# Optimization experiments

Measured on AMD Instinct MI355X. Metric: run time of the kernel, lower is better.

Reference implementation:

```python
import jax, jax.numpy as jnp
import numpy as np

NUM_ITERATIONS = 3


def squash(s, axis):
    # s: capsule vectors; squash along `axis` (capsule dim)
    mag_sq = jnp.sum(s * s, axis=axis, keepdims=True)
    mag = jnp.sqrt(mag_sq)
    return mag_sq / (1.0 + mag_sq) * (s / mag)


def setup_inputs() -> dict:
    key = jax.random.key(0)
    k1, k2 = jax.random.split(key)
    B, IN_SIZE, I = 256, 8, 1152   # batch, in_size, in_node_num
    N, O = 10, 16                  # num_node, node_size
    x = jax.random.normal(k1, (B, IN_SIZE, I), dtype=jnp.float32)
    W = jax.random.normal(k2, (1, I, N, O, IN_SIZE), dtype=jnp.float32)
    return {"x": x, "W": W}


def reference(x, W):
    # x: (B, in_size, I); W: (1, I, N, O, in_size)
    B = x.shape[0]
    I, N = W.shape[1], W.shape[2]
    xt = jnp.swapaxes(x, 1, 2)  # (B, I, in_size)
    # u_hat[b,i,n,o] = sum_k (0.03*W[0,i,n,o,k]) * x[b,i,k]
    u_hat = jnp.einsum('inok,bik->bino', W[0] * 0.03, xt)  # (B, I, N, O)
    b_ij = jnp.zeros((I, N), dtype=x.dtype)
    v_j = None
    for _ in range(NUM_ITERATIONS):
        c_ij = jax.nn.softmax(b_ij, axis=1)              # softmax over num_node
        s_j = jnp.einsum('in,bino->bno', c_ij, u_hat)    # (B, N, O)
        v_j = squash(s_j, axis=-1)                       # squash over node_size
        # agreement: u_hat . v_j, averaged over batch
        u_vj = jnp.einsum('bino,bno->bin', u_hat, v_j).mean(axis=0)  # (I, N)
        b_ij = b_ij + u_vj
    return v_j[:, :, :, None]  # (B, N, O, 1) == v_j.squeeze(1) in torch
```

## Files before the change

kernel.cpp:

```cpp
#include <hip/hip_runtime.h>

#define B_   256
#define I_   1152
#define N_   10
#define P_   9216
#define NO_  160

typedef unsigned short u16;
typedef short s8v __attribute__((ext_vector_type(8)));
typedef float f4v __attribute__((ext_vector_type(4)));

__device__ inline float bf2f(u16 u){
  unsigned v = ((unsigned)u) << 16; float f; __builtin_memcpy(&f, &v, 4); return f;
}
__device__ inline u16 f2bf(float f){
  unsigned b; __builtin_memcpy(&b, &f, 4);
  b += 0x7fffu + ((b >> 16) & 1u);
  return (u16)(b >> 16);
}

__global__ void k_prep(const float* __restrict__ x, const float* __restrict__ W,
                       u16* __restrict__ xbp, u16* __restrict__ xpb,
                       u16* __restrict__ Wt, u16* __restrict__ At,
                       float* __restrict__ bij){
  __shared__ float tile[32][36];
  int t = threadIdx.x, u = blockIdx.x;
  if (u < 160){
    if (u < 45) bij[u*256 + t] = 0.f;
    int q = u, n = q >> 4, o = q & 15;
    for (int i0 = 0; i0 < I_; i0 += 256){
      int i = i0 + t;
      if (i < I_){
        const float* src = W + (size_t)i*1280 + n*128 + o*8;
        float4 a = *reinterpret_cast<const float4*>(src);
        float4 b = *reinterpret_cast<const float4*>(src + 4);
        float vv[8] = {a.x,a.y,a.z,a.w,b.x,b.y,b.z,b.w};
        #pragma unroll
        for (int k = 0; k < 8; ++k){
          size_t addr = (size_t)q*P_ + (size_t)k*I_ + i;
          float wv = vv[k] * 0.03f;
          Wt[addr] = f2bf(wv);
          At[addr] = f2bf(wv * 0.1f);
        }
      }
    }
  } else {
    int b2 = u - 160;
    int tb = b2 & 7, tp = b2 >> 3;
    int b0 = tb << 5, p0 = tp << 5;
    int r = t >> 3, c4 = (t & 7) << 2;
    float4 v = *reinterpret_cast<const float4*>(x + (size_t)(b0 + r)*P_ + p0 + c4);
    *reinterpret_cast<float4*>(&tile[r][c4]) = v;
    uint2 pk;
    pk.x = (unsigned)f2bf(v.x) | ((unsigned)f2bf(v.y) << 16);
    pk.y = (unsigned)f2bf(v.z) | ((unsigned)f2bf(v.w) << 16);
    *reinterpret_cast<uint2*>(xbp + (size_t)(b0 + r)*P_ + p0 + c4) = pk;
    __syncthreads();
    float f0 = tile[c4+0][r], f1 = tile[c4+1][r], f2 = tile[c4+2][r], f3 = tile[c4+3][r];
    uint2 pk2;
    pk2.x = (unsigned)f2bf(f0) | ((unsigned)f2bf(f1) << 16);
    pk2.y = (unsigned)f2bf(f2) | ((unsigned)f2bf(f3) << 16);
    *reinterpret_cast<uint2*>(xpb + (size_t)(p0 + r)*B_ + b0 + c4) = pk2;
  }
}

__global__ void k_s(const u16* __restrict__ xbp, const u16* __restrict__ At,
                    float* __restrict__ s_part){
  int l = threadIdx.x;
  int b0 = blockIdx.x << 4;
  int n  = blockIdx.y;
  int kc = blockIdx.z;
  int lo = l & 15, quad = l >> 4;
  const s8v* ap = reinterpret_cast<const s8v*>(xbp + (size_t)(b0 + lo)*P_ + kc*576 + quad*8);
  const s8v* bp = reinterpret_cast<const s8v*>(At  + (size_t)(n*16 + lo)*P_ + kc*576 + quad*8);
  f4v acc0 = {0.f,0.f,0.f,0.f}, acc1 = {0.f,0.f,0.f,0.f};
  #pragma unroll
  for (int s = 0; s < 9; ++s){
    s8v a0 = ap[8*s],     b0v = bp[8*s];
    s8v a1 = ap[8*s + 4], b1v = bp[8*s + 4];
    acc0 = __builtin_amdgcn_mfma_f32_16x16x32_bf16(a0, b0v, acc0, 0, 0, 0);
    acc1 = __builtin_amdgcn_mfma_f32_16x16x32_bf16(a1, b1v, acc1, 0, 0, 0);
  }
  f4v acc = acc0 + acc1;
  float* op = s_part + (size_t)kc*40960;
  int r0 = quad << 2;
  #pragma unroll
  for (int r = 0; r < 4; ++r)
    op[(size_t)(b0 + r0 + r)*NO_ + n*16 + lo] = acc[r];
}

__global__ void k_sq(const float* __restrict__ s_part, float* __restrict__ out,
                     u16* __restrict__ vbt){
  int t = threadIdx.x;
  int o = t & 15, rl = t >> 4;
  int rowid = blockIdx.x*16 + rl;
  int b = rowid / 10, n = rowid - b*10;
  size_t idx = (size_t)b*NO_ + n*16 + o;
  float sv = 0.f;
  #pragma unroll
  for (int c = 0; c < 16; ++c) sv += s_part[idx + (size_t)c*40960];
  float sq = sv * sv;
  #pragma unroll
  for (int m = 8; m >= 1; m >>= 1) sq += __shfl_xor(sq, m, 16);
  float outv = sv * sqrtf(sq) / (1.0f + sq);
  out[idx] = outv;
  vbt[(size_t)(n*16 + o)*B_ + b] = f2bf(outv);
}

__global__ void k_g(const u16* __restrict__ xpb, const u16* __restrict__ vbt,
                    const u16* __restrict__ Wt, float* __restrict__ bij){
  int w = blockIdx.x*4 + (threadIdx.x >> 6);
  int l = threadIdx.x & 63;
  int pt = w % 576, qp = w / 576;
  int p0 = pt << 4;
  int lo = l & 15, quad = l >> 4;
  const s8v* ap  = reinterpret_cast<const s8v*>(xpb + (size_t)(p0 + lo)*B_ + quad*8);
  const s8v* bp0 = reinterpret_cast<const s8v*>(vbt + (size_t)((qp*2+0)*16 + lo)*B_ + quad*8);
  const s8v* bp1 = reinterpret_cast<const s8v*>(vbt + (size_t)((qp*2+1)*16 + lo)*B_ + quad*8);
  f4v acc0 = {0.f,0.f,0.f,0.f}, acc1 = {0.f,0.f,0.f,0.f};
  #pragma unroll
  for (int s = 0; s < 8; ++s){
    s8v a  = ap[4*s];
    s8v b0 = bp0[4*s];
    s8v b1 = bp1[4*s];
    acc0 = __builtin_amdgcn_mfma_f32_16x16x32_bf16(a, b0, acc0, 0, 0, 0);
    acc1 = __builtin_amdgcn_mfma_f32_16x16x32_bf16(a, b1, acc1, 0, 0, 0);
  }
  int ib = p0 % 1152;
  #pragma unroll
  for (int s = 0; s < 2; ++s){
    f4v acc = s ? acc1 : acc0;
    int n = qp*2 + s;
    const u16* wp = Wt + (size_t)(n*16 + lo)*P_ + p0 + (quad << 2);
    ushort4 w4 = *reinterpret_cast<const ushort4*>(wp);
    float v0 = acc[0]*bf2f(w4.x), v1 = acc[1]*bf2f(w4.y);
    float v2 = acc[2]*bf2f(w4.z), v3 = acc[3]*bf2f(w4.w);
    #pragma unroll
    for (int m = 8; m >= 1; m >>= 1){
      v0 += __shfl_xor(v0, m, 16);
      v1 += __shfl_xor(v1, m, 16);
      v2 += __shfl_xor(v2, m, 16);
      v3 += __shfl_xor(v3, m, 16);
    }
    if (lo == 0){
      int i = ib + (quad << 2);
      atomicAdd(&bij[(i+0)*N_ + n], v0 * (1.f/256.f));
      atomicAdd(&bij[(i+1)*N_ + n], v1 * (1.f/256.f));
      atomicAdd(&bij[(i+2)*N_ + n], v2 * (1.f/256.f));
      atomicAdd(&bij[(i+3)*N_ + n], v3 * (1.f/256.f));
    }
  }
}

__global__ void k_at(const float* __restrict__ bij, const u16* __restrict__ Wt,
                     u16* __restrict__ At){
  __shared__ float c_pad[I_];
  int t = threadIdx.x, u = blockIdx.x;
  int n = u / 72;
  for (int i = t; i < I_; i += 256){
    const float* br = bij + i*N_;
    float l0 = br[0], l1 = br[1], l2 = br[2], l3 = br[3], l4 = br[4];
    float l5 = br[5], l6 = br[6], l7 = br[7], l8 = br[8], l9 = br[9];
    float mx = fmaxf(fmaxf(fmaxf(fmaxf(l0,l1),fmaxf(l2,l3)),
                           fmaxf(fmaxf(l4,l5),fmaxf(l6,l7))), fmaxf(l8,l9));
    float e0=__expf(l0-mx), e1=__expf(l1-mx), e2=__expf(l2-mx), e3=__expf(l3-mx), e4=__expf(l4-mx);
    float e5=__expf(l5-mx), e6=__expf(l6-mx), e7=__expf(l7-mx), e8=__expf(l8-mx), e9=__expf(l9-mx);
    float se = e0+e1+e2+e3+e4+e5+e6+e7+e8+e9;
    float ev[10] = {e0,e1,e2,e3,e4,e5,e6,e7,e8,e9};
    c_pad[i] = ev[n] / se;
  }
  __syncthreads();
  int base = (u*256 + t) * 8;
  int rem = base % P_;
  int i0 = rem % I_;
  uint4 w = *reinterpret_cast<const uint4*>(Wt + base);
  float4 c0 = *reinterpret_cast<const float4*>(&c_pad[i0]);
  float4 c1 = *reinterpret_cast<const float4*>(&c_pad[i0 + 4]);
  uint4 r;
  r.x = (unsigned)f2bf(bf2f(w.x & 0xffff) * c0.x) | ((unsigned)f2bf(bf2f(w.x >> 16) * c0.y) << 16);
  r.y = (unsigned)f2bf(bf2f(w.y & 0xffff) * c0.z) | ((unsigned)f2bf(bf2f(w.y >> 16) * c0.w) << 16);
  r.z = (unsigned)f2bf(bf2f(w.z & 0xffff) * c1.x) | ((unsigned)f2bf(bf2f(w.z >> 16) * c1.y) << 16);
  r.w = (unsigned)f2bf(bf2f(w.w & 0xffff) * c1.z) | ((unsigned)f2bf(bf2f(w.w >> 16) * c1.w) << 16);
  *reinterpret_cast<uint4*>(At + base) = r;
}

extern "C" void kernel_launch(void* const* d_in, const int* in_sizes, int n_in,
                              void* d_out, int out_size, void* d_ws, size_t ws_size,
                              hipStream_t stream){
  (void)in_sizes; (void)n_in; (void)out_size; (void)ws_size;
  const float* x = (const float*)d_in[0];
  const float* W = (const float*)d_in[1];
  float* out = (float*)d_out;

  float* s_part = (float*)d_ws;
  float* bij    = s_part + 16*40960;
  u16* xbp = (u16*)(bij + 11520);
  u16* xpb = xbp + 2359296;
  u16* Wt  = xpb + 2359296;
  u16* At  = Wt  + 1474560;
  u16* vbt = At  + 1474560;

  k_prep<<<2464, 256, 0, stream>>>(x, W, xbp, xpb, Wt, At, bij);
  for (int it = 0; it < 3; ++it){
    if (it > 0){
      k_g<<<720, 256, 0, stream>>>(xpb, vbt, Wt, bij);
      k_at<<<720, 256, 0, stream>>>(bij, Wt, At);
    }
    k_s<<<dim3(16, 10, 16), 64, 0, stream>>>(xbp, At, s_part);
    k_sq<<<160, 256, 0, stream>>>(s_part, out, vbt);
  }
}
```

Baseline: 152.5 us.

## Fuse softmax-weighted W scaling into the s-projection kernel, drop k_at

Removes the separate k_at kernel and the At buffer. Each k_s2 block now computes the softmax coefficients for its 576-row i-range from bij, scales its Wt slice into shared memory, and then runs the MFMA reduction with B operands read from LDS. This drops two launches and the global write and re-read of At. In exchange, each block recomputes softmax, and blocks now use 2 waves each to amortise that work. On the first iteration bij is zero, so the computed coefficient is 0.1, matching the old prescaled At.

New measurement: 143.2 us. 6.1% less time.

```diff
diff --git a/kernel.cpp b/kernel.cpp
--- a/kernel.cpp
+++ b/kernel.cpp
@@ -21,8 +21,7 @@
 
 __global__ void k_prep(const float* __restrict__ x, const float* __restrict__ W,
                        u16* __restrict__ xbp, u16* __restrict__ xpb,
-                       u16* __restrict__ Wt, u16* __restrict__ At,
-                       float* __restrict__ bij){
+                       u16* __restrict__ Wt, float* __restrict__ bij){
   __shared__ float tile[32][36];
   int t = threadIdx.x, u = blockIdx.x;
   if (u < 160){
@@ -36,12 +35,8 @@
         float4 b = *reinterpret_cast<const float4*>(src + 4);
         float vv[8] = {a.x,a.y,a.z,a.w,b.x,b.y,b.z,b.w};
         #pragma unroll
-        for (int k = 0; k < 8; ++k){
-          size_t addr = (size_t)q*P_ + (size_t)k*I_ + i;
-          float wv = vv[k] * 0.03f;
-          Wt[addr] = f2bf(wv);
-          At[addr] = f2bf(wv * 0.1f);
-        }
+        for (int k = 0; k < 8; ++k)
+          Wt[(size_t)q*P_ + (size_t)k*I_ + i] = f2bf(vv[k] * 0.03f);
       }
     }
   } else {
@@ -64,20 +59,54 @@
   }
 }
 
-__global__ void k_s(const u16* __restrict__ xbp, const u16* __restrict__ At,
-                    float* __restrict__ s_part){
-  int l = threadIdx.x;
-  int b0 = blockIdx.x << 4;
-  int n  = blockIdx.y;
-  int kc = blockIdx.z;
+__global__ __launch_bounds__(128) void k_s2(
+    const u16* __restrict__ xbp, const u16* __restrict__ Wt,
+    const float* __restrict__ bij, float* __restrict__ s_part){
+  __shared__ u16  Bt[16][584];
+  __shared__ float c_lds[576];
+  int t = threadIdx.x;
+  int bx2 = blockIdx.x, n = blockIdx.y, kc = blockIdx.z;
+  int i0 = (kc & 1) * 576;
+
+  for (int j = t; j < 576; j += 128){
+    const float* br = bij + (size_t)(i0 + j)*N_;
+    float l0 = br[0], l1 = br[1], l2 = br[2], l3 = br[3], l4 = br[4];
+    float l5 = br[5], l6 = br[6], l7 = br[7], l8 = br[8], l9 = br[9];
+    float mx = fmaxf(fmaxf(fmaxf(fmaxf(l0,l1),fmaxf(l2,l3)),
+                           fmaxf(fmaxf(l4,l5),fmaxf(l6,l7))), fmaxf(l8,l9));
+    float e0=__expf(l0-mx), e1=__expf(l1-mx), e2=__expf(l2-mx), e3=__expf(l3-mx), e4=__expf(l4-mx);
+    float e5=__expf(l5-mx), e6=__expf(l6-mx), e7=__expf(l7-mx), e8=__expf(l8-mx), e9=__expf(l9-mx);
+    float se = e0+e1+e2+e3+e4+e5+e6+e7+e8+e9;
+    float ev[10] = {e0,e1,e2,e3,e4,e5,e6,e7,e8,e9};
+    c_lds[j] = ev[n] / se;
+  }
+  __syncthreads();
+
+  for (int u = t; u < 1152; u += 128){
+    int r = u / 72, cb = (u - r*72) * 8;
+    uint4 w = *reinterpret_cast<const uint4*>(Wt + (size_t)(n*16 + r)*P_ + kc*576 + cb);
+    float4 c0 = *reinterpret_cast<const float4*>(&c_lds[cb]);
+    float4 c1 = *reinterpret_cast<const float4*>(&c_lds[cb + 4]);
+    uint4 rr;
+    rr.x = (unsigned)f2bf(bf2f(w.x & 0xffff)*c0.x) | ((unsigned)f2bf(bf2f(w.x >> 16)*c0.y) << 16);
+    rr.y = (unsigned)f2bf(bf2f(w.y & 0xffff)*c0.z) | ((unsigned)f2bf(bf2f(w.y >> 16)*c0.w) << 16);
+    rr.z = (unsigned)f2bf(bf2f(w.z & 0xffff)*c1.x) | ((unsigned)f2bf(bf2f(w.z >> 16)*c1.y) << 16);
+    rr.w = (unsigned)f2bf(bf2f(w.w & 0xffff)*c1.z) | ((unsigned)f2bf(bf2f(w.w >> 16)*c1.w) << 16);
+    *reinterpret_cast<uint4*>(&Bt[r][cb]) = rr;
+  }
+  __syncthreads();
+
+  int w = t >> 6, l = t & 63;
   int lo = l & 15, quad = l >> 4;
+  int b0 = bx2*32 + w*16;
   const s8v* ap = reinterpret_cast<const s8v*>(xbp + (size_t)(b0 + lo)*P_ + kc*576 + quad*8);
-  const s8v* bp = reinterpret_cast<const s8v*>(At  + (size_t)(n*16 + lo)*P_ + kc*576 + quad*8);
   f4v acc0 = {0.f,0.f,0.f,0.f}, acc1 = {0.f,0.f,0.f,0.f};
   #pragma unroll
   for (int s = 0; s < 9; ++s){
-    s8v a0 = ap[8*s],     b0v = bp[8*s];
-    s8v a1 = ap[8*s + 4], b1v = bp[8*s + 4];
+    s8v a0 = ap[8*s];
+    s8v b0v = *reinterpret_cast<const s8v*>(&Bt[lo][quad*8 + 64*s]);
+    s8v a1 = ap[8*s + 4];
+    s8v b1v = *reinterpret_cast<const s8v*>(&Bt[lo][quad*8 + 64*s + 32]);
     acc0 = __builtin_amdgcn_mfma_f32_16x16x32_bf16(a0, b0v, acc0, 0, 0, 0);
     acc1 = __builtin_amdgcn_mfma_f32_16x16x32_bf16(a1, b1v, acc1, 0, 0, 0);
   }
@@ -152,38 +181,6 @@
   }
 }
 
-__global__ void k_at(const float* __restrict__ bij, const u16* __restrict__ Wt,
-                     u16* __restrict__ At){
-  __shared__ float c_pad[I_];
-  int t = threadIdx.x, u = blockIdx.x;
-  int n = u / 72;
-  for (int i = t; i < I_; i += 256){
-    const float* br = bij + i*N_;
-    float l0 = br[0], l1 = br[1], l2 = br[2], l3 = br[3], l4 = br[4];
-    float l5 = br[5], l6 = br[6], l7 = br[7], l8 = br[8], l9 = br[9];
-    float mx = fmaxf(fmaxf(fmaxf(fmaxf(l0,l1),fmaxf(l2,l3)),
-                           fmaxf(fmaxf(l4,l5),fmaxf(l6,l7))), fmaxf(l8,l9));
-    float e0=__expf(l0-mx), e1=__expf(l1-mx), e2=__expf(l2-mx), e3=__expf(l3-mx), e4=__expf(l4-mx);
-    float e5=__expf(l5-mx), e6=__expf(l6-mx), e7=__expf(l7-mx), e8=__expf(l8-mx), e9=__expf(l9-mx);
-    float se = e0+e1+e2+e3+e4+e5+e6+e7+e8+e9;
-    float ev[10] = {e0,e1,e2,e3,e4,e5,e6,e7,e8,e9};
-    c_pad[i] = ev[n] / se;
-  }
-  __syncthreads();
-  int base = (u*256 + t) * 8;
-  int rem = base % P_;
-  int i0 = rem % I_;
-  uint4 w = *reinterpret_cast<const uint4*>(Wt + base);
-  float4 c0 = *reinterpret_cast<const float4*>(&c_pad[i0]);
-  float4 c1 = *reinterpret_cast<const float4*>(&c_pad[i0 + 4]);
-  uint4 r;
-  r.x = (unsigned)f2bf(bf2f(w.x & 0xffff) * c0.x) | ((unsigned)f2bf(bf2f(w.x >> 16) * c0.y) << 16);
-  r.y = (unsigned)f2bf(bf2f(w.y & 0xffff) * c0.z) | ((unsigned)f2bf(bf2f(w.y >> 16) * c0.w) << 16);
-  r.z = (unsigned)f2bf(bf2f(w.z & 0xffff) * c1.x) | ((unsigned)f2bf(bf2f(w.z >> 16) * c1.y) << 16);
-  r.w = (unsigned)f2bf(bf2f(w.w & 0xffff) * c1.z) | ((unsigned)f2bf(bf2f(w.w >> 16) * c1.w) << 16);
-  *reinterpret_cast<uint4*>(At + base) = r;
-}
-
 extern "C" void kernel_launch(void* const* d_in, const int* in_sizes, int n_in,
                               void* d_out, int out_size, void* d_ws, size_t ws_size,
                               hipStream_t stream){
@@ -197,16 +194,13 @@
   u16* xbp = (u16*)(bij + 11520);
   u16* xpb = xbp + 2359296;
   u16* Wt  = xpb + 2359296;
-  u16* At  = Wt  + 1474560;
-  u16* vbt = At  + 1474560;
-
-  k_prep<<<2464, 256, 0, stream>>>(x, W, xbp, xpb, Wt, At, bij);
+  u16* vbt = Wt  + 1474560;
+
+  k_prep<<<2464, 256, 0, stream>>>(x, W, xbp, xpb, Wt, bij);
   for (int it = 0; it < 3; ++it){
-    if (it > 0){
+    k_s2<<<dim3(8, 10, 16), 128, 0, stream>>>(xbp, Wt, bij, s_part);
+    k_sq<<<160, 256, 0, stream>>>(s_part, out, vbt);
+    if (it < 2)
       k_g<<<720, 256, 0, stream>>>(xpb, vbt, Wt, bij);
-      k_at<<<720, 256, 0, stream>>>(bij, Wt, At);
-    }
-    k_s<<<dim3(16, 10, 16), 64, 0, stream>>>(xbp, At, s_part);
-    k_sq<<<160, 256, 0, stream>>>(s_part, out, vbt);
-  }
-}
+  }
+}
```
